# Performance work log

Hardware: AMD Instinct MI355X
Metric: run time of the kernel (lower is better)

The kernel has to match this reference:

```python
import jax, jax.numpy as jnp
import numpy as np

B, S, D, M, E, K = 2, 2048, 1024, 1408, 8, 2  # batch, seq, n_embed, n_moe_mlp, n_experts, top_k


def setup_inputs() -> dict:
    key = jax.random.key(0)
    k0, k1, k2, k3, k4 = jax.random.split(key, 5)
    scale = 0.02
    return {
        "x": jax.random.normal(k0, (B, S, D), dtype=jnp.float32),
        "w_gate": jax.random.normal(k1, (D, E), dtype=jnp.float32) * scale,  # gate.weight.T
        "w_g": jax.random.normal(k2, (E, D, M), dtype=jnp.float32) * scale,  # gate_proj.weight.T per expert
        "w_u": jax.random.normal(k3, (E, D, M), dtype=jnp.float32) * scale,  # up_proj.weight.T per expert
        "w_d": jax.random.normal(k4, (E, M, D), dtype=jnp.float32) * scale,  # down_proj.weight.T per expert
    }


def reference(x, w_gate, w_g, w_u, w_d):
    # router
    scores = x @ w_gate                                  # [B,S,E]
    topk_scores, topk_idx = jax.lax.top_k(scores, K)     # [B,S,K]
    topk_probs = jax.nn.softmax(topk_scores, axis=-1)    # softmax over selected experts only
    # scatter top-k probs back to dense [B,S,E] gating (top_k indices are distinct)
    gating = jnp.sum(
        jax.nn.one_hot(topk_idx, E, dtype=topk_probs.dtype) * topk_probs[..., None],
        axis=-2,
    )                                                    # [B,S,E]
    # dense all-expert SwiGLU (faithful to the compute-then-mask original)
    hidden = jax.nn.silu(jnp.einsum("bsd,edm->ebsm", x, w_g)) * jnp.einsum(
        "bsd,edm->ebsm", x, w_u
    )                                                    # [E,B,S,M]
    expert_out = jnp.einsum("ebsm,emd->ebsd", hidden, w_d)  # [E,B,S,D]
    # masked weighted combine
    y = jnp.einsum("bse,ebsd->bsd", gating, expert_out)  # [B,S,D]
    return y
```

## Files before the change

kernel.cpp:

```cpp
#include <hip/hip_runtime.h>
#include <cstdio>

constexpr int T  = 4096;
constexpr int D  = 1024;
constexpr int M  = 1408;
constexpr int E  = 8;

constexpr int TM = 128;
constexpr int TN = 128;
constexpr int BK = 32;
constexpr int RCAP = T * 2 + E * TM;
constexpr int MT_MAX = T / TM;
constexpr int NT_UP = M / TN;
constexpr int NT_DN = D / TN;

constexpr int CSTR = 64;
constexpr int TOKB = 16;
constexpr int RTB  = T / TOKB;
constexpr int XCV  = (T * D) / 2048;
constexpr int TPW  = E * (D / 64) * (M / 64);
constexpr int PREP_GRID = RTB + XCV + 2 * TPW;
constexpr int NGEMM_UP  = E * MT_MAX * NT_UP;
constexpr int UPG_GRID  = NGEMM_UP + TPW;

typedef _Float16 half8 __attribute__((ext_vector_type(8)));
typedef _Float16 half4 __attribute__((ext_vector_type(4)));
typedef float    floatx4 __attribute__((ext_vector_type(4)));

#define VMW12() asm volatile("s_waitcnt vmcnt(12)" ::: "memory")
#define VMW8()  asm volatile("s_waitcnt vmcnt(8)"  ::: "memory")
#define VMW6()  asm volatile("s_waitcnt vmcnt(6)"  ::: "memory")
#define VMW4()  asm volatile("s_waitcnt vmcnt(4)"  ::: "memory")
#define VMW0()  asm volatile("s_waitcnt vmcnt(0)"  ::: "memory")

constexpr size_t OFF_COUNTS = 0;
constexpr size_t OFF_BASE   = (size_t)E * CSTR * 4;
constexpr size_t OFF_PC     = OFF_BASE + 64;
constexpr size_t OFF_TOTAL  = OFF_PC + 64;
constexpr size_t OFF_T2E    = OFF_TOTAL + 64;
constexpr size_t OFF_T2POS  = OFF_T2E   + (size_t)2 * T * 4;
constexpr size_t OFF_T2P    = OFF_T2POS + (size_t)2 * T * 4;
constexpr size_t OFF_TLIST  = OFF_T2P   + (size_t)2 * T * 4;
constexpr size_t OFF_XG     = OFF_TLIST + (size_t)E * T * 4;
constexpr size_t OFF_HID    = OFF_XG  + (size_t)RCAP * D * 2;
constexpr size_t OFF_WGT    = OFF_HID + (size_t)RCAP * M * 2;
constexpr size_t OFF_WUT    = OFF_WGT + (size_t)E * M * D * 2;
constexpr size_t OFF_WDT    = OFF_WUT + (size_t)E * M * D * 2;
constexpr size_t WS_NEED    = OFF_WDT + (size_t)E * D * M * 2;

__device__ __forceinline__ void gl_lds16(const void* g, void* l) {
  __builtin_amdgcn_global_load_lds(
      (const __attribute__((address_space(1))) unsigned int*)g,
      (__attribute__((address_space(3))) unsigned int*)l, 16, 0, 0);
}

__device__ __forceinline__ void expert_base_pc(const int* __restrict__ counts,
                                               int e, int& base_e, int& pc_e,
                                               int& cnt_e) {
  int b = 0; base_e = 0; pc_e = 0; cnt_e = 0;
  #pragma unroll
  for (int ee = 0; ee < E; ++ee) {
    int c = counts[ee * CSTR];
    int p = (c + TM - 1) / TM * TM;
    if (ee == e) { base_e = b; pc_e = p; cnt_e = c; }
    b += p;
  }
}

__device__ __forceinline__ void transpose64(
    const float* __restrict__ src, _Float16* __restrict__ dst,
    int Rr, int Cc, int j, float (*tile)[69]) {
  int ctn = Cc >> 6, rtn = Rr >> 6;
  int e   = j / (ctn * rtn);
  int rem = j - e * (ctn * rtn);
  int rt = rem / ctn, ct = rem - rt * ctn;
  int t = threadIdx.x;
  int lr = t >> 2;
  int lc = (t & 3) * 16;
  const float* s = src + ((size_t)e * Rr + rt * 64 + lr) * Cc + ct * 64 + lc;
  float4 v0 = *(const float4*)(s + 0);
  float4 v1 = *(const float4*)(s + 4);
  float4 v2 = *(const float4*)(s + 8);
  float4 v3 = *(const float4*)(s + 12);
  float* tr = &tile[lr][lc];
  tr[0]  = v0.x; tr[1]  = v0.y; tr[2]  = v0.z; tr[3]  = v0.w;
  tr[4]  = v1.x; tr[5]  = v1.y; tr[6]  = v1.z; tr[7]  = v1.w;
  tr[8]  = v2.x; tr[9]  = v2.y; tr[10] = v2.z; tr[11] = v2.w;
  tr[12] = v3.x; tr[13] = v3.y; tr[14] = v3.z; tr[15] = v3.w;
  __syncthreads();
  #pragma unroll
  for (int rep = 0; rep < 2; ++rep) {
    int s2 = t + rep * 256;
    int oc = s2 >> 3;
    int sl = s2 & 7;
    half8 o;
    #pragma unroll
    for (int q = 0; q < 8; ++q) o[q] = (_Float16)tile[sl * 8 + q][oc];
    *(half8*)(dst + ((size_t)e * Cc + ct * 64 + oc) * Rr + rt * 64 + sl * 8) = o;
  }
}

__global__ __launch_bounds__(256) void k_prep(
    const float* __restrict__ x, const float* __restrict__ wgate,
    const float* __restrict__ w_g, const float* __restrict__ w_u,
    _Float16* __restrict__ Xh,
    _Float16* __restrict__ wgT, _Float16* __restrict__ wuT,
    int* __restrict__ counts, int* __restrict__ tlist,
    int* __restrict__ t2e, int* __restrict__ t2pos, float* __restrict__ t2p) {
  __shared__ float tile[64][69];
  __shared__ int   s_cnt[E];
  __shared__ int   s_base[E];
  __shared__ int   s_e[2 * TOKB];
  __shared__ int   s_pos[2 * TOKB];
  __shared__ float s_p[2 * TOKB];
  int bid = blockIdx.x;

  if (bid < RTB) {
    int wv = threadIdx.x >> 6, lane = threadIdx.x & 63;
    if (threadIdx.x < E) s_cnt[threadIdx.x] = 0;
    __syncthreads();
    for (int j = 0; j < TOKB / 4; ++j) {
      int tl = wv * (TOKB / 4) + j;
      int t  = bid * TOKB + tl;
      const float* xr = x + (size_t)t * D;
      float acc[E] = {0.f,0.f,0.f,0.f,0.f,0.f,0.f,0.f};
      #pragma unroll
      for (int i = 0; i < D / 64; ++i) {
        int d = i * 64 + lane;
        float xv = xr[d];
        const float4* wr2 = (const float4*)(wgate + (size_t)d * E);
        float4 w0 = wr2[0], w1 = wr2[1];
        acc[0] += xv * w0.x; acc[1] += xv * w0.y; acc[2] += xv * w0.z; acc[3] += xv * w0.w;
        acc[4] += xv * w1.x; acc[5] += xv * w1.y; acc[6] += xv * w1.z; acc[7] += xv * w1.w;
      }
      #pragma unroll
      for (int e = 0; e < E; ++e) {
        #pragma unroll
        for (int off = 32; off; off >>= 1) acc[e] += __shfl_xor(acc[e], off, 64);
      }
      if (lane == 0) {
        int i0 = 0; float s0 = acc[0];
        #pragma unroll
        for (int e = 1; e < E; ++e) if (acc[e] > s0) { s0 = acc[e]; i0 = e; }
        int i1 = -1; float s1 = -1e30f;
        #pragma unroll
        for (int e = 0; e < E; ++e) if (e != i0 && acc[e] > s1) { s1 = acc[e]; i1 = e; }
        float p0 = 1.f / (1.f + expf(s1 - s0));
        float p1 = 1.f - p0;
        int q0 = atomicAdd(&s_cnt[i0], 1);
        int q1 = atomicAdd(&s_cnt[i1], 1);
        s_e[2 * tl]     = i0; s_pos[2 * tl]     = q0; s_p[2 * tl]     = p0;
        s_e[2 * tl + 1] = i1; s_pos[2 * tl + 1] = q1; s_p[2 * tl + 1] = p1;
      }
    }
    __syncthreads();
    if (threadIdx.x < E)
      s_base[threadIdx.x] = atomicAdd(&counts[threadIdx.x * CSTR], s_cnt[threadIdx.x]);
    __syncthreads();
    if (threadIdx.x < 2 * TOKB) {
      int sl = threadIdx.x;
      int e = s_e[sl];
      int pos = s_base[e] + s_pos[sl];
      int t = bid * TOKB + (sl >> 1);
      tlist[e * T + pos] = t;
      t2e[2 * t + (sl & 1)]   = e;
      t2pos[2 * t + (sl & 1)] = pos;
      t2p[2 * t + (sl & 1)]   = s_p[sl];
    }
    return;
  }

  if (bid < RTB + XCV) {
    size_t base = (size_t)(bid - RTB) * 2048 + threadIdx.x * 8;
    float4 v0 = *(const float4*)(x + base);
    float4 v1 = *(const float4*)(x + base + 4);
    half8 h;
    h[0] = (_Float16)v0.x; h[1] = (_Float16)v0.y;
    h[2] = (_Float16)v0.z; h[3] = (_Float16)v0.w;
    h[4] = (_Float16)v1.x; h[5] = (_Float16)v1.y;
    h[6] = (_Float16)v1.z; h[7] = (_Float16)v1.w;
    *(half8*)(Xh + base) = h;
    return;
  }

  int i = bid - RTB - XCV;
  if (i < TPW) transpose64(w_g, wgT, D, M, i, tile);
  else         transpose64(w_u, wuT, D, M, i - TPW, tile);
}

__global__ __launch_bounds__(256, 2) void k_upgate(
    const _Float16* __restrict__ Xh, const _Float16* __restrict__ wgT,
    const _Float16* __restrict__ wuT, _Float16* __restrict__ Hid,
    const int* __restrict__ counts, const int* __restrict__ tlist,
    const float* __restrict__ w_d, _Float16* __restrict__ wdT) {
  __shared__ _Float16 As[3][TM * BK];
  __shared__ _Float16 Bg[3][TN * BK];
  __shared__ _Float16 Bu[3][TN * BK];
  int lin = blockIdx.x;
  if (lin >= NGEMM_UP) {
    float (*tile)[69] = reinterpret_cast<float (*)[69]>(&As[0][0]);
    transpose64(w_d, wdT, M, D, lin - NGEMM_UP, tile);
    return;
  }
  int e = lin & 7;
  int r = lin >> 3;
  int nt = r % NT_UP;
  int mt = r / NT_UP;
  int base_e, pc_e, cnt_e;
  expert_base_pc(counts, e, base_e, pc_e, cnt_e);
  if (mt * TM >= pc_e) return;
  int row0 = base_e + mt * TM;
  int n0 = nt * TN;
  int tid = threadIdx.x;
  int w = tid >> 6, lane = tid & 63;
  int lrow = lane & 15, quad = lane >> 4;
  int wr = w >> 1, wc = w & 1;
  int sr = lane >> 2;
  int c4 = lane & 3;
  int swc = ((c4 ^ ((sr >> 1) & 3))) * 8;

  const _Float16* wg_e = wgT + (size_t)e * M * D;
  const _Float16* wu_e = wuT + (size_t)e * M * D;
  const _Float16* pA[2]; const _Float16* pG[2]; const _Float16* pU[2];
  int loff[2];
  #pragma unroll
  for (int is = 0; is < 2; ++is) {
    int grow = w * 32 + is * 16 + sr;
    int local = mt * TM + grow;
    int trow = (local < cnt_e) ? tlist[e * T + local] : 0;
    pA[is] = Xh   + (size_t)trow * D + swc;
    pG[is] = wg_e + (size_t)(n0 + grow) * D + swc;
    pU[is] = wu_e + (size_t)(n0 + grow) * D + swc;
    loff[is] = (w * 2 + is) * 1024;
  }

  int swr = (lrow >> 1) & 3;

  floatx4 accg[4][4] = {};
  floatx4 accu[4][4] = {};

  auto stage = [&](int b) {
    char* a0 = (char*)&As[b][0];
    char* g0 = (char*)&Bg[b][0];
    char* u0 = (char*)&Bu[b][0];
    #pragma unroll
    for (int is = 0; is < 2; ++is) {
      gl_lds16(pA[is], a0 + loff[is]); pA[is] += BK;
      gl_lds16(pG[is], g0 + loff[is]); pG[is] += BK;
      gl_lds16(pU[is], u0 + loff[is]); pU[is] += BK;
    }
  };
  auto compute = [&](int b) {
    int kc = (quad ^ swr) * 8;
    half8 af[4];
    #pragma unroll
    for (int i = 0; i < 4; ++i)
      af[i] = *(const half8*)&As[b][(wr * 64 + i * 16 + lrow) * BK + kc];
    #pragma unroll
    for (int c = 0; c < 4; ++c) {
      int bo = (wc * 64 + c * 16 + lrow) * BK + kc;
      half8 bgc = *(const half8*)&Bg[b][bo];
      half8 buc = *(const half8*)&Bu[b][bo];
      #pragma unroll
      for (int i = 0; i < 4; ++i) {
        accg[c][i] = __builtin_amdgcn_mfma_f32_16x16x32_f16(af[i], bgc, accg[c][i], 0, 0, 0);
        accu[c][i] = __builtin_amdgcn_mfma_f32_16x16x32_f16(af[i], buc, accu[c][i], 0, 0, 0);
      }
    }
  };

  constexpr int NTK = D / BK;
  stage(0); stage(1);
  for (int k = 0; k < NTK; ++k) {
    if (k + 2 < NTK) {
      stage((k + 2) % 3);
      VMW12();
    } else if (k + 1 < NTK) {
      VMW6();
    } else {
      VMW0();
    }
    __builtin_amdgcn_sched_barrier(0);
    __builtin_amdgcn_s_barrier();
    compute(k % 3);
    __builtin_amdgcn_s_barrier();
  }

  #pragma unroll
  for (int c = 0; c < 4; ++c) {
    int col = n0 + wc * 64 + c * 16 + lrow;
    #pragma unroll
    for (int i = 0; i < 4; ++i) {
      int rowb = row0 + wr * 64 + i * 16 + quad * 4;
      #pragma unroll
      for (int reg = 0; reg < 4; ++reg) {
        float g = accg[c][i][reg], u = accu[c][i][reg];
        Hid[(size_t)(rowb + reg) * M + col] = (_Float16)(g / (1.f + expf(-g)) * u);
      }
    }
  }
}

__global__ __launch_bounds__(256, 2) void k_down(
    const _Float16* __restrict__ Hid, const _Float16* __restrict__ wdT,
    _Float16* __restrict__ Yp, const int* __restrict__ counts) {
  int lin = blockIdx.x;
  int e = lin & 7;
  int r = lin >> 3;
  int nt = r % NT_DN;
  int mt = r / NT_DN;
  int base_e, pc_e, cnt_e;
  expert_base_pc(counts, e, base_e, pc_e, cnt_e);
  if (mt * TM >= pc_e) return;
  int row0 = base_e + mt * TM;
  int d0 = nt * TN;
  __shared__ _Float16 As[3][TM * BK];
  __shared__ _Float16 Bs[3][TN * BK];
  int tid = threadIdx.x;
  int w = tid >> 6, lane = tid & 63;
  int lrow = lane & 15, quad = lane >> 4;
  int wr = w >> 1, wc = w & 1;
  int sr = lane >> 2;
  int c4 = lane & 3;
  int swc = ((c4 ^ ((sr >> 1) & 3))) * 8;

  const _Float16* wd_e = wdT + (size_t)e * D * M;
  const _Float16* pA[2]; const _Float16* pB[2];
  int loff[2];
  #pragma unroll
  for (int is = 0; is < 2; ++is) {
    int grow = w * 32 + is * 16 + sr;
    pA[is] = Hid  + (size_t)(row0 + grow) * M + swc;
    pB[is] = wd_e + (size_t)(d0   + grow) * M + swc;
    loff[is] = (w * 2 + is) * 1024;
  }

  int swr = (lrow >> 1) & 3;

  floatx4 acc[4][4] = {};

  auto stage = [&](int b) {
    char* a0 = (char*)&As[b][0];
    char* b0 = (char*)&Bs[b][0];
    #pragma unroll
    for (int is = 0; is < 2; ++is) {
      gl_lds16(pA[is], a0 + loff[is]); pA[is] += BK;
      gl_lds16(pB[is], b0 + loff[is]); pB[is] += BK;
    }
  };
  auto compute = [&](int b) {
    int kc = (quad ^ swr) * 8;
    half8 af[4];
    #pragma unroll
    for (int i = 0; i < 4; ++i)
      af[i] = *(const half8*)&As[b][(wr * 64 + i * 16 + lrow) * BK + kc];
    #pragma unroll
    for (int c = 0; c < 4; ++c) {
      half8 bc = *(const half8*)&Bs[b][(wc * 64 + c * 16 + lrow) * BK + kc];
      #pragma unroll
      for (int i = 0; i < 4; ++i)
        acc[c][i] = __builtin_amdgcn_mfma_f32_16x16x32_f16(af[i], bc, acc[c][i], 0, 0, 0);
    }
  };

  constexpr int NTK = M / BK;
  stage(0); stage(1);
  for (int k = 0; k < NTK; ++k) {
    if (k + 2 < NTK) {
      stage((k + 2) % 3);
      VMW8();
    } else if (k + 1 < NTK) {
      VMW4();
    } else {
      VMW0();
    }
    __builtin_amdgcn_sched_barrier(0);
    __builtin_amdgcn_s_barrier();
    compute(k % 3);
    __builtin_amdgcn_s_barrier();
  }

  #pragma unroll
  for (int c = 0; c < 4; ++c) {
    int col = d0 + wc * 64 + c * 16 + lrow;
    #pragma unroll
    for (int i = 0; i < 4; ++i) {
      int rowb = row0 + wr * 64 + i * 16 + quad * 4;
      #pragma unroll
      for (int reg = 0; reg < 4; ++reg)
        Yp[(size_t)(rowb + reg) * D + col] = (_Float16)acc[c][i][reg];
    }
  }
}

__global__ __launch_bounds__(256) void k_combine(
    const _Float16* __restrict__ Yp, const int* __restrict__ counts,
    const int* __restrict__ t2e, const int* __restrict__ t2pos,
    const float* __restrict__ t2p, float* __restrict__ out) {
  int t = blockIdx.x;
  int e0 = t2e[2 * t], e1 = t2e[2 * t + 1];
  int b = 0, b0 = 0, b1 = 0;
  #pragma unroll
  for (int ee = 0; ee < E; ++ee) {
    if (ee == e0) b0 = b;
    if (ee == e1) b1 = b;
    int c = counts[ee * CSTR];
    b += (c + TM - 1) / TM * TM;
  }
  int r0 = b0 + t2pos[2 * t];
  int r1 = b1 + t2pos[2 * t + 1];
  float p0 = t2p[2 * t], p1 = t2p[2 * t + 1];
  int d = threadIdx.x * 4;
  half4 h0 = *(const half4*)(Yp + (size_t)r0 * D + d);
  half4 h1 = *(const half4*)(Yp + (size_t)r1 * D + d);
  float4 o;
  o.x = p0 * (float)h0.x + p1 * (float)h1.x;
  o.y = p0 * (float)h0.y + p1 * (float)h1.y;
  o.z = p0 * (float)h0.z + p1 * (float)h1.z;
  o.w = p0 * (float)h0.w + p1 * (float)h1.w;
  *(float4*)(out + (size_t)t * D + d) = o;
}

extern "C" void kernel_launch(void* const* d_in, const int* in_sizes, int n_in,
                              void* d_out, int out_size, void* d_ws, size_t ws_size,
                              hipStream_t stream) {
  const float* x     = (const float*)d_in[0];
  const float* wgate = (const float*)d_in[1];
  const float* w_g   = (const float*)d_in[2];
  const float* w_u   = (const float*)d_in[3];
  const float* w_d   = (const float*)d_in[4];
  float* out = (float*)d_out;
  char* ws = (char*)d_ws;

  if (ws_size < WS_NEED) {
    fprintf(stderr, "kernel_launch: ws_size=%zu < needed %zu\n", ws_size, WS_NEED);
    return;
  }

  int* counts = (int*)(ws + OFF_COUNTS);
  int* t2e    = (int*)(ws + OFF_T2E);
  int* t2pos  = (int*)(ws + OFF_T2POS);
  float* t2p  = (float*)(ws + OFF_T2P);
  int* tlist  = (int*)(ws + OFF_TLIST);
  _Float16* Xh  = (_Float16*)(ws + OFF_XG);
  _Float16* Hid = (_Float16*)(ws + OFF_HID);
  _Float16* wgT = (_Float16*)(ws + OFF_WGT);
  _Float16* wuT = (_Float16*)(ws + OFF_WUT);
  _Float16* wdT = (_Float16*)(ws + OFF_WDT);

  hipMemsetAsync(counts, 0, (size_t)E * CSTR * 4, stream);

  k_prep<<<PREP_GRID, 256, 0, stream>>>(x, wgate, w_g, w_u, Xh,
                                        wgT, wuT,
                                        counts, tlist, t2e, t2pos, t2p);
  k_upgate<<<UPG_GRID, 256, 0, stream>>>(Xh, wgT, wuT, Hid, counts, tlist,
                                         w_d, wdT);
  _Float16* Yp = Xh;
  k_down<<<E * MT_MAX * NT_DN, 256, 0, stream>>>(Hid, wdT, Yp, counts);
  k_combine<<<T, 256, 0, stream>>>(Yp, counts, t2e, t2pos, t2p, out);
}
```

Measured before the change: 288.5 us.

## Fuse combine into down GEMM via atomics and merge router into fp16 convert

```diff
diff --git a/kernel.cpp b/kernel.cpp
--- a/kernel.cpp
+++ b/kernel.cpp
@@ -9,40 +9,31 @@
 constexpr int TM = 128;
 constexpr int TN = 128;
 constexpr int BK = 32;
-constexpr int RCAP = T * 2 + E * TM;
 constexpr int MT_MAX = T / TM;
 constexpr int NT_UP = M / TN;
 constexpr int NT_DN = D / TN;
+constexpr int RCAP = T * 2 + E * TM;
 
 constexpr int CSTR = 64;
-constexpr int TOKB = 16;
-constexpr int RTB  = T / TOKB;
-constexpr int XCV  = (T * D) / 2048;
+constexpr int XCV  = T / 2;
 constexpr int TPW  = E * (D / 64) * (M / 64);
-constexpr int PREP_GRID = RTB + XCV + 2 * TPW;
+constexpr int PREP_GRID = XCV + 2 * TPW;
 constexpr int NGEMM_UP  = E * MT_MAX * NT_UP;
 constexpr int UPG_GRID  = NGEMM_UP + TPW;
 
 typedef _Float16 half8 __attribute__((ext_vector_type(8)));
-typedef _Float16 half4 __attribute__((ext_vector_type(4)));
 typedef float    floatx4 __attribute__((ext_vector_type(4)));
 
 #define VMW12() asm volatile("s_waitcnt vmcnt(12)" ::: "memory")
-#define VMW8()  asm volatile("s_waitcnt vmcnt(8)"  ::: "memory")
 #define VMW6()  asm volatile("s_waitcnt vmcnt(6)"  ::: "memory")
 #define VMW4()  asm volatile("s_waitcnt vmcnt(4)"  ::: "memory")
 #define VMW0()  asm volatile("s_waitcnt vmcnt(0)"  ::: "memory")
 
 constexpr size_t OFF_COUNTS = 0;
-constexpr size_t OFF_BASE   = (size_t)E * CSTR * 4;
-constexpr size_t OFF_PC     = OFF_BASE + 64;
-constexpr size_t OFF_TOTAL  = OFF_PC + 64;
-constexpr size_t OFF_T2E    = OFF_TOTAL + 64;
-constexpr size_t OFF_T2POS  = OFF_T2E   + (size_t)2 * T * 4;
-constexpr size_t OFF_T2P    = OFF_T2POS + (size_t)2 * T * 4;
-constexpr size_t OFF_TLIST  = OFF_T2P   + (size_t)2 * T * 4;
-constexpr size_t OFF_XG     = OFF_TLIST + (size_t)E * T * 4;
-constexpr size_t OFF_HID    = OFF_XG  + (size_t)RCAP * D * 2;
+constexpr size_t OFF_TLIST  = 2048;
+constexpr size_t OFF_PLIST  = OFF_TLIST + (size_t)E * T * 4;
+constexpr size_t OFF_XH     = OFF_PLIST + (size_t)E * T * 4;
+constexpr size_t OFF_HID    = OFF_XH  + (size_t)T * D * 2;
 constexpr size_t OFF_WGT    = OFF_HID + (size_t)RCAP * M * 2;
 constexpr size_t OFF_WUT    = OFF_WGT + (size_t)E * M * D * 2;
 constexpr size_t OFF_WDT    = OFF_WUT + (size_t)E * M * D * 2;
@@ -106,84 +97,69 @@
     _Float16* __restrict__ Xh,
     _Float16* __restrict__ wgT, _Float16* __restrict__ wuT,
     int* __restrict__ counts, int* __restrict__ tlist,
-    int* __restrict__ t2e, int* __restrict__ t2pos, float* __restrict__ t2p) {
+    float* __restrict__ plist) {
   __shared__ float tile[64][69];
-  __shared__ int   s_cnt[E];
-  __shared__ int   s_base[E];
-  __shared__ int   s_e[2 * TOKB];
-  __shared__ int   s_pos[2 * TOKB];
-  __shared__ float s_p[2 * TOKB];
+  __shared__ float s_red[4][8];
   int bid = blockIdx.x;
 
-  if (bid < RTB) {
-    int wv = threadIdx.x >> 6, lane = threadIdx.x & 63;
-    if (threadIdx.x < E) s_cnt[threadIdx.x] = 0;
-    __syncthreads();
-    for (int j = 0; j < TOKB / 4; ++j) {
-      int tl = wv * (TOKB / 4) + j;
-      int t  = bid * TOKB + tl;
-      const float* xr = x + (size_t)t * D;
-      float acc[E] = {0.f,0.f,0.f,0.f,0.f,0.f,0.f,0.f};
-      #pragma unroll
-      for (int i = 0; i < D / 64; ++i) {
-        int d = i * 64 + lane;
-        float xv = xr[d];
-        const float4* wr2 = (const float4*)(wgate + (size_t)d * E);
-        float4 w0 = wr2[0], w1 = wr2[1];
-        acc[0] += xv * w0.x; acc[1] += xv * w0.y; acc[2] += xv * w0.z; acc[3] += xv * w0.w;
-        acc[4] += xv * w1.x; acc[5] += xv * w1.y; acc[6] += xv * w1.z; acc[7] += xv * w1.w;
-      }
-      #pragma unroll
-      for (int e = 0; e < E; ++e) {
-        #pragma unroll
-        for (int off = 32; off; off >>= 1) acc[e] += __shfl_xor(acc[e], off, 64);
-      }
-      if (lane == 0) {
-        int i0 = 0; float s0 = acc[0];
-        #pragma unroll
-        for (int e = 1; e < E; ++e) if (acc[e] > s0) { s0 = acc[e]; i0 = e; }
-        int i1 = -1; float s1 = -1e30f;
-        #pragma unroll
-        for (int e = 0; e < E; ++e) if (e != i0 && acc[e] > s1) { s1 = acc[e]; i1 = e; }
-        float p0 = 1.f / (1.f + expf(s1 - s0));
-        float p1 = 1.f - p0;
-        int q0 = atomicAdd(&s_cnt[i0], 1);
-        int q1 = atomicAdd(&s_cnt[i1], 1);
-        s_e[2 * tl]     = i0; s_pos[2 * tl]     = q0; s_p[2 * tl]     = p0;
-        s_e[2 * tl + 1] = i1; s_pos[2 * tl + 1] = q1; s_p[2 * tl + 1] = p1;
-      }
-    }
-    __syncthreads();
-    if (threadIdx.x < E)
-      s_base[threadIdx.x] = atomicAdd(&counts[threadIdx.x * CSTR], s_cnt[threadIdx.x]);
-    __syncthreads();
-    if (threadIdx.x < 2 * TOKB) {
-      int sl = threadIdx.x;
-      int e = s_e[sl];
-      int pos = s_base[e] + s_pos[sl];
-      int t = bid * TOKB + (sl >> 1);
-      tlist[e * T + pos] = t;
-      t2e[2 * t + (sl & 1)]   = e;
-      t2pos[2 * t + (sl & 1)] = pos;
-      t2p[2 * t + (sl & 1)]   = s_p[sl];
-    }
-    return;
-  }
-
-  if (bid < RTB + XCV) {
-    size_t base = (size_t)(bid - RTB) * 2048 + threadIdx.x * 8;
-    float4 v0 = *(const float4*)(x + base);
-    float4 v1 = *(const float4*)(x + base + 4);
+  if (bid < XCV) {
+    int tid = threadIdx.x;
+    int row  = tid >> 7;
+    int t    = bid * 2 + row;
+    int dpos = (tid & 127) * 8;
+    int wv = tid >> 6, lane = tid & 63;
+    const float* xr = x + (size_t)t * D + dpos;
+    float4 v0 = *(const float4*)(xr);
+    float4 v1 = *(const float4*)(xr + 4);
     half8 h;
     h[0] = (_Float16)v0.x; h[1] = (_Float16)v0.y;
     h[2] = (_Float16)v0.z; h[3] = (_Float16)v0.w;
     h[4] = (_Float16)v1.x; h[5] = (_Float16)v1.y;
     h[6] = (_Float16)v1.z; h[7] = (_Float16)v1.w;
-    *(half8*)(Xh + base) = h;
+    *(half8*)(Xh + (size_t)t * D + dpos) = h;
+    float xv[8] = {v0.x, v0.y, v0.z, v0.w, v1.x, v1.y, v1.z, v1.w};
+    float acc[8] = {0.f,0.f,0.f,0.f,0.f,0.f,0.f,0.f};
+    #pragma unroll
+    for (int j = 0; j < 8; ++j) {
+      const float4* wr2 = (const float4*)(wgate + (size_t)(dpos + j) * E);
+      float4 w0 = wr2[0], w1 = wr2[1];
+      acc[0] += xv[j] * w0.x; acc[1] += xv[j] * w0.y;
+      acc[2] += xv[j] * w0.z; acc[3] += xv[j] * w0.w;
+      acc[4] += xv[j] * w1.x; acc[5] += xv[j] * w1.y;
+      acc[6] += xv[j] * w1.z; acc[7] += xv[j] * w1.w;
+    }
+    #pragma unroll
+    for (int e = 0; e < 8; ++e) {
+      #pragma unroll
+      for (int off = 32; off; off >>= 1) acc[e] += __shfl_xor(acc[e], off, 64);
+    }
+    if (lane == 0) {
+      #pragma unroll
+      for (int e = 0; e < 8; ++e) s_red[wv][e] = acc[e];
+    }
+    __syncthreads();
+    if ((tid & 127) == 0) {
+      int wb = row * 2;
+      float sc[8];
+      #pragma unroll
+      for (int e = 0; e < 8; ++e) sc[e] = s_red[wb][e] + s_red[wb + 1][e];
+      int i0 = 0; float s0 = sc[0];
+      #pragma unroll
+      for (int e = 1; e < 8; ++e) if (sc[e] > s0) { s0 = sc[e]; i0 = e; }
+      int i1 = -1; float s1 = -1e30f;
+      #pragma unroll
+      for (int e = 0; e < 8; ++e) if (e != i0 && sc[e] > s1) { s1 = sc[e]; i1 = e; }
+      float p0 = 1.f / (1.f + expf(s1 - s0));
+      float p1 = 1.f - p0;
+      int q0 = atomicAdd(&counts[i0 * CSTR], 1);
+      int q1 = atomicAdd(&counts[i1 * CSTR], 1);
+      tlist[i0 * T + q0] = t; plist[i0 * T + q0] = p0;
+      tlist[i1 * T + q1] = t; plist[i1 * T + q1] = p1;
+    }
     return;
   }
 
-  int i = bid - RTB - XCV;
+  int i = bid - XCV;
   if (i < TPW) transpose64(w_g, wgT, D, M, i, tile);
   else         transpose64(w_u, wuT, D, M, i - TPW, tile);
 }
@@ -301,9 +277,10 @@
   }
 }
 
-__global__ __launch_bounds__(256, 2) void k_down(
+__global__ __launch_bounds__(256, 3) void k_down(
     const _Float16* __restrict__ Hid, const _Float16* __restrict__ wdT,
-    _Float16* __restrict__ Yp, const int* __restrict__ counts) {
+    float* __restrict__ out, const int* __restrict__ counts,
+    const int* __restrict__ tlist, const float* __restrict__ plist) {
   int lin = blockIdx.x;
   int e = lin & 7;
   int r = lin >> 3;
@@ -314,8 +291,8 @@
   if (mt * TM >= pc_e) return;
   int row0 = base_e + mt * TM;
   int d0 = nt * TN;
-  __shared__ _Float16 As[3][TM * BK];
-  __shared__ _Float16 Bs[3][TN * BK];
+  __shared__ _Float16 As[2][TM * BK];
+  __shared__ _Float16 Bs[2][TN * BK];
   int tid = threadIdx.x;
   int w = tid >> 6, lane = tid & 63;
   int lrow = lane & 15, quad = lane >> 4;
@@ -364,61 +341,45 @@
   };
 
   constexpr int NTK = M / BK;
-  stage(0); stage(1);
+  stage(0);
+  int cur = 0;
   for (int k = 0; k < NTK; ++k) {
-    if (k + 2 < NTK) {
-      stage((k + 2) % 3);
-      VMW8();
-    } else if (k + 1 < NTK) {
+    if (k + 1 < NTK) {
+      stage(cur ^ 1);
       VMW4();
     } else {
       VMW0();
     }
     __builtin_amdgcn_sched_barrier(0);
     __builtin_amdgcn_s_barrier();
-    compute(k % 3);
+    compute(cur);
     __builtin_amdgcn_s_barrier();
-  }
-
+    cur ^= 1;
+  }
+
+  int tI[4][4]; float pI[4][4];
+  #pragma unroll
+  for (int i = 0; i < 4; ++i) {
+    #pragma unroll
+    for (int reg = 0; reg < 4; ++reg) {
+      int rl = mt * TM + wr * 64 + i * 16 + quad * 4 + reg;
+      bool valid = rl < cnt_e;
+      tI[i][reg] = valid ? tlist[e * T + rl] : -1;
+      pI[i][reg] = valid ? plist[e * T + rl] : 0.f;
+    }
+  }
   #pragma unroll
   for (int c = 0; c < 4; ++c) {
     int col = d0 + wc * 64 + c * 16 + lrow;
     #pragma unroll
     for (int i = 0; i < 4; ++i) {
-      int rowb = row0 + wr * 64 + i * 16 + quad * 4;
-      #pragma unroll
-      for (int reg = 0; reg < 4; ++reg)
-        Yp[(size_t)(rowb + reg) * D + col] = (_Float16)acc[c][i][reg];
-    }
-  }
-}
-
-__global__ __launch_bounds__(256) void k_combine(
-    const _Float16* __restrict__ Yp, const int* __restrict__ counts,
-    const int* __restrict__ t2e, const int* __restrict__ t2pos,
-    const float* __restrict__ t2p, float* __restrict__ out) {
-  int t = blockIdx.x;
-  int e0 = t2e[2 * t], e1 = t2e[2 * t + 1];
-  int b = 0, b0 = 0, b1 = 0;
-  #pragma unroll
-  for (int ee = 0; ee < E; ++ee) {
-    if (ee == e0) b0 = b;
-    if (ee == e1) b1 = b;
-    int c = counts[ee * CSTR];
-    b += (c + TM - 1) / TM * TM;
-  }
-  int r0 = b0 + t2pos[2 * t];
-  int r1 = b1 + t2pos[2 * t + 1];
-  float p0 = t2p[2 * t], p1 = t2p[2 * t + 1];
-  int d = threadIdx.x * 4;
-  half4 h0 = *(const half4*)(Yp + (size_t)r0 * D + d);
-  half4 h1 = *(const half4*)(Yp + (size_t)r1 * D + d);
-  float4 o;
-  o.x = p0 * (float)h0.x + p1 * (float)h1.x;
-  o.y = p0 * (float)h0.y + p1 * (float)h1.y;
-  o.z = p0 * (float)h0.z + p1 * (float)h1.z;
-  o.w = p0 * (float)h0.w + p1 * (float)h1.w;
-  *(float4*)(out + (size_t)t * D + d) = o;
+      #pragma unroll
+      for (int reg = 0; reg < 4; ++reg) {
+        if (tI[i][reg] >= 0)
+          atomicAdd(&out[(size_t)tI[i][reg] * D + col], pI[i][reg] * acc[c][i][reg]);
+      }
+    }
+  }
 }
 
 extern "C" void kernel_launch(void* const* d_in, const int* in_sizes, int n_in,
@@ -437,25 +398,22 @@
     return;
   }
 
-  int* counts = (int*)(ws + OFF_COUNTS);
-  int* t2e    = (int*)(ws + OFF_T2E);
-  int* t2pos  = (int*)(ws + OFF_T2POS);
-  float* t2p  = (float*)(ws + OFF_T2P);
-  int* tlist  = (int*)(ws + OFF_TLIST);
-  _Float16* Xh  = (_Float16*)(ws + OFF_XG);
+  int* counts   = (int*)(ws + OFF_COUNTS);
+  int* tlist    = (int*)(ws + OFF_TLIST);
+  float* plist  = (float*)(ws + OFF_PLIST);
+  _Float16* Xh  = (_Float16*)(ws + OFF_XH);
   _Float16* Hid = (_Float16*)(ws + OFF_HID);
   _Float16* wgT = (_Float16*)(ws + OFF_WGT);
   _Float16* wuT = (_Float16*)(ws + OFF_WUT);
   _Float16* wdT = (_Float16*)(ws + OFF_WDT);
 
   hipMemsetAsync(counts, 0, (size_t)E * CSTR * 4, stream);
+  hipMemsetAsync(out, 0, (size_t)T * D * 4, stream);
 
   k_prep<<<PREP_GRID, 256, 0, stream>>>(x, wgate, w_g, w_u, Xh,
-                                        wgT, wuT,
-                                        counts, tlist, t2e, t2pos, t2p);
+                                        wgT, wuT, counts, tlist, plist);
   k_upgate<<<UPG_GRID, 256, 0, stream>>>(Xh, wgT, wuT, Hid, counts, tlist,
                                          w_d, wdT);
-  _Float16* Yp = Xh;
-  k_down<<<E * MT_MAX * NT_DN, 256, 0, stream>>>(Hid, wdT, Yp, counts);
-  k_combine<<<T, 256, 0, stream>>>(Yp, counts, t2e, t2pos, t2p, out);
-}
+  k_down<<<E * MT_MAX * NT_DN, 256, 0, stream>>>(Hid, wdT, out, counts,
+                                                 tlist, plist);
+}
```

Result: slower. 327.5 us (+13.5%).
